# Kernel optimization log

Measured on AMD Instinct MI355X. Metric: run time of the kernel, lower is better.

Reference implementation:

```python
import jax, jax.numpy as jnp
import numpy as np

B, T, D, H = 4, 1024, 1024, 16
TP = 1024
HD = D // H
LN_EPS = 1e-3  # keras LayerNormalization default epsilon


def snac_linear(x, wt, mt):
    # conv1dsnac: w = tanh(wt) * sigmoid(mt), shape [1, nx, nf] -> [nx, nf]
    w = (jnp.tanh(wt) * jax.nn.sigmoid(mt))[0]
    return jnp.einsum('btx,xf->btf', x, w)


def layernorm(x, gamma, beta):
    mu = jnp.mean(x, axis=-1, keepdims=True)
    var = jnp.mean(jnp.square(x - mu), axis=-1, keepdims=True)
    return (x - mu) * jax.lax.rsqrt(var + LN_EPS) * gamma + beta


def setup_inputs() -> dict:
    key = jax.random.key(0)
    ks = jax.random.split(key, 10)
    s = 0.02
    return {
        'input': jax.random.normal(ks[0], (B, T, D), jnp.float32),
        'past': jax.random.normal(ks[1], (B, 2, H, TP, HD), jnp.float32),
        'qkv_wt': jax.random.normal(ks[2], (1, D, 3 * D), jnp.float32) * s,
        'qkv_mt': jax.random.normal(ks[3], (1, D, 3 * D), jnp.float32) * s,
        'merge_wt': jax.random.normal(ks[4], (1, D, D), jnp.float32) * s,
        'merge_mt': jax.random.normal(ks[5], (1, D, D), jnp.float32) * s,
        'ln1_wt': jax.random.normal(ks[6], (1, D, D), jnp.float32) * s,
        'ln1_mt': jax.random.normal(ks[7], (1, D, D), jnp.float32) * s,
        'g1': jnp.ones((D,), jnp.float32), 'b1': jnp.zeros((D,), jnp.float32),
        'g2': jnp.ones((D,), jnp.float32), 'b2': jnp.zeros((D,), jnp.float32),
    }


def reference(input, past, qkv_wt, qkv_mt, merge_wt, merge_mt, ln1_wt, ln1_mt, g1, b1, g2, b2):
    x = input
    xn = layernorm(x, g1, b1)
    c = snac_linear(xn, qkv_wt, qkv_mt)  # [B, T, 3D]
    q, k, v = jnp.split(c, 3, axis=2)
    # split heads -> [B, H, T, HD]
    to_heads = lambda t: t.reshape(B, T, H, HD).transpose(0, 2, 1, 3)
    q, k, v = to_heads(q), to_heads(k), to_heads(v)
    present = jnp.stack([k, v], axis=1)  # [B, 2, H, T, HD]
    pk, pv = past[:, 0], past[:, 1]
    k = jnp.concatenate([pk, k], axis=2)  # [B, H, TP+T, HD]
    v = jnp.concatenate([pv, v], axis=2)
    nd, ns = T, TP + T
    w = jnp.einsum('bhqd,bhkd->bhqk', q, k) * jax.lax.rsqrt(jnp.float32(HD))
    i = jnp.arange(nd)[:, None]
    j = jnp.arange(ns)[None, :]
    m = (i >= j - ns + nd).astype(w.dtype)  # [nd, ns] causal mask incl. past
    w = w * m - jnp.asarray(1e10, w.dtype) * (1 - m)
    msk = jax.nn.softmax(w, axis=-1)  # [B, H, T, TP+T]
    a = jnp.einsum('bhqk,bhkd->bhqd', msk, v)
    ah = a.transpose(0, 2, 1, 3).reshape(B, T, D)  # merge heads
    am = snac_linear(ah, merge_wt, merge_mt)
    xa = x + am
    mlp = snac_linear(layernorm(xa, g2, b2), ln1_wt, ln1_mt)
    xm = xa + mlp
    return xm, present, msk
```

## Files before the change

### kernel.cpp

```cpp
#include <hip/hip_runtime.h>
#include <hip/hip_bf16.h>

typedef _Float16 half8 __attribute__((ext_vector_type(8)));
typedef _Float16 half4v __attribute__((ext_vector_type(4)));
typedef float f32x4 __attribute__((ext_vector_type(4)));

#define DEV static __device__ __forceinline__


typedef __attribute__((address_space(1))) const unsigned int* gas_p;
typedef __attribute__((address_space(3))) unsigned int* las_p;
DEV void glds16(const void* g, void* s) {
  __builtin_amdgcn_global_load_lds((gas_p)g, (las_p)s, 16, 0, 0);
}

__global__ __launch_bounds__(256) void prep_all(const float* __restrict__ qkv_wt,
                                                const float* __restrict__ qkv_mt,
                                                const float* __restrict__ mg_wt,
                                                const float* __restrict__ mg_mt,
                                                const float* __restrict__ l1_wt,
                                                const float* __restrict__ l1_mt,
                                                _Float16* __restrict__ wq,
                                                _Float16* __restrict__ wm,
                                                _Float16* __restrict__ wl) {
  __shared__ float tile[64][65];
  const float *wt, *mt;
  _Float16* out;
  int N, bid;
  if (blockIdx.x < 768) {
    wt = qkv_wt; mt = qkv_mt; out = wq; N = 3072; bid = blockIdx.x;
  } else if (blockIdx.x < 1024) {
    wt = mg_wt; mt = mg_mt; out = wm; N = 1024; bid = blockIdx.x - 768;
  } else {
    wt = l1_wt; mt = l1_mt; out = wl; N = 1024; bid = blockIdx.x - 1024;
  }
  const int ntiles = N >> 6;
  const int nt = bid % ntiles, kt = bid / ntiles;
  const int k0 = kt << 6, n0 = nt << 6;
  const int t = threadIdx.x, r = t >> 2, c0 = (t & 3) << 4;
  const long ibase = (long)(k0 + r) * N + n0 + c0;
#pragma unroll
  for (int j = 0; j < 16; j += 4) {
    float4 a = *(const float4*)(wt + ibase + j);
    float4 b = *(const float4*)(mt + ibase + j);
    tile[r][c0 + j + 0] = tanhf(a.x) / (1.f + __expf(-b.x));
    tile[r][c0 + j + 1] = tanhf(a.y) / (1.f + __expf(-b.y));
    tile[r][c0 + j + 2] = tanhf(a.z) / (1.f + __expf(-b.z));
    tile[r][c0 + j + 3] = tanhf(a.w) / (1.f + __expf(-b.w));
  }
  __syncthreads();
  half8 o0, o1;
#pragma unroll
  for (int j = 0; j < 8; ++j) {
    o0[j] = (_Float16)tile[c0 + j][r];
    o1[j] = (_Float16)tile[c0 + 8 + j][r];
  }
  _Float16* dst = out + (long)(n0 + r) * 1024 + k0 + c0;
  *(half8*)dst = o0;
  *(half8*)(dst + 8) = o1;
}

__global__ __launch_bounds__(256) void kv_prep(const float* __restrict__ past,
                                               const _Float16* __restrict__ vnew,
                                               _Float16* __restrict__ kf,
                                               _Float16* __restrict__ vt) {
  __shared__ float tile[64][65];
  if (blockIdx.x < 4096) {
    const long e = ((long)blockIdx.x * 256 + threadIdx.x) * 4;
    const int b = (int)(e >> 20);
    const int rem = (int)(e & 1048575);
    float4 v = *(const float4*)(past + (long)b * 2097152 + rem);
    half4v o = {(_Float16)v.x, (_Float16)v.y, (_Float16)v.z, (_Float16)v.w};
    const int h = rem >> 16, td = rem & 65535;
    *(half4v*)(kf + (long)(b * 16 + h) * 131072 + td) = o;
    return;
  }
  const int bid = blockIdx.x - 4096;
  const int bh = bid >> 5, kt = bid & 31;
  const int b = bh >> 4, h = bh & 15;
  const int k0 = kt << 6;
  const int t = threadIdx.x, r = t >> 2, c0 = (t & 3) << 4;
  if (k0 < 1024) {
    const float* src = past + (((long)(b * 2 + 1) * 16 + h) * 1024 + (k0 + r)) * 64 + c0;
#pragma unroll
    for (int j = 0; j < 16; j += 4) {
      float4 v = *(const float4*)(src + j);
      tile[r][c0 + j + 0] = v.x;
      tile[r][c0 + j + 1] = v.y;
      tile[r][c0 + j + 2] = v.z;
      tile[r][c0 + j + 3] = v.w;
    }
  } else {
    const _Float16* src = vnew + ((long)bh * 1024 + (k0 - 1024 + r)) * 64 + c0;
    half8 a = *(const half8*)src;
    half8 bq = *(const half8*)(src + 8);
#pragma unroll
    for (int j = 0; j < 8; ++j) {
      tile[r][c0 + j] = (float)a[j];
      tile[r][c0 + 8 + j] = (float)bq[j];
    }
  }
  __syncthreads();
  half8 o0, o1;
#pragma unroll
  for (int j = 0; j < 8; ++j) {
    o0[j] = (_Float16)tile[c0 + j][r];
    o1[j] = (_Float16)tile[c0 + 8 + j][r];
  }
  _Float16* dst = vt + ((long)bh * 64 + r) * 2048 + k0 + c0;
  *(half8*)dst = o0;
  *(half8*)(dst + 8) = o1;
}

__global__ __launch_bounds__(256) void ln_k(const float* __restrict__ x,
                                            const float* __restrict__ g,
                                            const float* __restrict__ be,
                                            _Float16* __restrict__ out) {
  __shared__ float red[4];
  const int row = blockIdx.x, tid = threadIdx.x, l = tid & 63, w = tid >> 6;
  float4 v = *(const float4*)(x + (long)row * 1024 + tid * 4);
  float s = v.x + v.y + v.z + v.w;
#pragma unroll
  for (int o = 32; o > 0; o >>= 1) s += __shfl_down(s, o, 64);
  if (l == 0) red[w] = s;
  __syncthreads();
  const float mu = (red[0] + red[1] + red[2] + red[3]) * (1.f / 1024.f);
  float dx = v.x - mu, dy = v.y - mu, dz = v.z - mu, dw = v.w - mu;
  float ss = dx * dx + dy * dy + dz * dz + dw * dw;
#pragma unroll
  for (int o = 32; o > 0; o >>= 1) ss += __shfl_down(ss, o, 64);
  __syncthreads();
  if (l == 0) red[w] = ss;
  __syncthreads();
  const float var = (red[0] + red[1] + red[2] + red[3]) * (1.f / 1024.f);
  const float rs = rsqrtf(var + 1e-3f);
  float4 gv = *(const float4*)(g + tid * 4);
  float4 bv = *(const float4*)(be + tid * 4);
  half4v o = {(_Float16)(dx * rs * gv.x + bv.x), (_Float16)(dy * rs * gv.y + bv.y),
              (_Float16)(dz * rs * gv.z + bv.z), (_Float16)(dw * rs * gv.w + bv.w)};
  *(half4v*)(out + (long)row * 1024 + tid * 4) = o;
}

template <int BM, int EPI>
__global__ __launch_bounds__(256) void gemm_k(const _Float16* __restrict__ A,
                                              const _Float16* __restrict__ Bt,
                                              int mtiles,
                                              _Float16* __restrict__ e_q,
                                              _Float16* __restrict__ e_k,
                                              _Float16* __restrict__ e_v,
                                              float* __restrict__ e_present,
                                              const float* __restrict__ e_res,
                                              float* __restrict__ e_out) {
  constexpr int FM = BM / 32;
  __shared__ __align__(16) char smem[2 * BM * 128 + 32768];
  char* Bbase = smem + 2 * BM * 128;
  const int tid = threadIdx.x, l = tid & 63, w = tid >> 6;
  const int wm = w >> 1, wn = w & 1;
  const int bm = blockIdx.x % mtiles, bn = blockIdx.x / mtiles;
  const long m0 = (long)bm * BM, n0 = (long)bn * 128;

  f32x4 acc[FM][4];
#pragma unroll
  for (int i = 0; i < FM; ++i)
#pragma unroll
    for (int j = 0; j < 4; ++j) acc[i][j] = (f32x4){0.f, 0.f, 0.f, 0.f};

  auto stage = [&](int b, int kt) {
#pragma unroll
    for (int i = 0; i < FM; ++i) {
      const int cid = i * 256 + tid, row = cid >> 3, u = cid & 7;
      glds16(A + (m0 + row) * 1024 + kt * 64 + ((u ^ (row & 7)) << 3),
             smem + b * BM * 128 + i * 4096 + w * 1024);
    }
#pragma unroll
    for (int i = 0; i < 4; ++i) {
      const int cid = i * 256 + tid, row = cid >> 3, u = cid & 7;
      glds16(Bt + (n0 + row) * 1024 + kt * 64 + ((u ^ (row & 7)) << 3),
             Bbase + b * 16384 + i * 4096 + w * 1024);
    }
  };

  stage(0, 0);
  __syncthreads();
  for (int kt = 0; kt < 16; ++kt) {
    const int cur = kt & 1;
    if (kt < 15) stage(cur ^ 1, kt + 1);
    const char* As = smem + cur * BM * 128;
    const char* Bs = Bbase + cur * 16384;
#pragma unroll
    for (int k2 = 0; k2 < 2; ++k2) {
      const int sl = k2 * 4 + (l >> 4);
      half8 bfr[4];
#pragma unroll
      for (int fn = 0; fn < 4; ++fn) {
        const int rn = wn * 64 + fn * 16 + (l & 15);
        bfr[fn] = *(const half8*)(Bs + rn * 128 + ((sl ^ (rn & 7)) << 4));
      }
#pragma unroll
      for (int fm = 0; fm < FM; ++fm) {
        const int rm = wm * (BM / 2) + fm * 16 + (l & 15);
        const half8 afr = *(const half8*)(As + rm * 128 + ((sl ^ (rm & 7)) << 4));
#pragma unroll
        for (int fn = 0; fn < 4; ++fn)
          acc[fm][fn] = __builtin_amdgcn_mfma_f32_16x16x32_f16(afr, bfr[fn], acc[fm][fn], 0, 0, 0);
      }
    }
    __syncthreads();
  }
#pragma unroll
  for (int fm = 0; fm < FM; ++fm) {
#pragma unroll
    for (int fn = 0; fn < 4; ++fn) {
#pragma unroll
      for (int r = 0; r < 4; ++r) {
        const long row = m0 + wm * (BM / 2) + fm * 16 + (l >> 4) * 4 + r;
        const long col = n0 + fn * 16 + (l & 15) + wn * 64;
        const float v = acc[fm][fn][r];
        if constexpr (EPI == 0) {
          const int b = (int)(row >> 10), t = (int)(row & 1023);
          const int sec = (int)(col >> 10), h = ((int)col >> 6) & 15, hd = (int)col & 63;
          const long bh = b * 16 + h;
          if (sec == 0) {
            e_q[(bh * 1024 + t) * 64 + hd] = (_Float16)v;
          } else if (sec == 1) {
            e_present[(((long)(b * 2) * 16 + h) * 1024 + t) * 64 + hd] = v;
            e_k[(bh * 2048 + 1024 + t) * 64 + hd] = (_Float16)v;
          } else {
            e_present[(((long)(b * 2 + 1) * 16 + h) * 1024 + t) * 64 + hd] = v;
            e_v[(bh * 1024 + t) * 64 + hd] = (_Float16)v;
          }
        } else {
          e_out[row * 1024 + col] = e_res[row * 1024 + col] + v;
        }
      }
    }
  }
}

__global__ __launch_bounds__(256, 4) void attn_k(const _Float16* __restrict__ qg,
                                                 const _Float16* __restrict__ kg,
                                                 const _Float16* __restrict__ vtg,
                                                 float* __restrict__ msk,
                                                 _Float16* __restrict__ ah) {
  __shared__ __align__(16) char smem[40960];
  char* ps_all = smem + 32768;
  const int tid = threadIdx.x, l = tid & 63, w = tid >> 6;
  char* psw = ps_all + w * 2048;
  const int lq = l & 15, hi = l >> 4;

  const int x = blockIdx.x & 7, g = blockIdx.x >> 3;
  const int bh = (g & 7) * 8 + x;
  const int qt = 15 - (g >> 3);
  const int r0 = qt << 6;
  const int nc = (r0 + 1151) >> 6;
  const int rowg0 = r0 + w * 16;

  const _Float16* kb = kg + (long)bh * 131072;
  const _Float16* vb = vtg + (long)bh * 131072;
  float* mskb = msk + ((long)bh * 1024 + rowg0) * 2048;

  half8 qa[2];
  {
    const _Float16* qp = qg + ((long)bh * 1024 + rowg0 + lq) * 64 + hi * 8;
    qa[0] = *(const half8*)qp;
    qa[1] = *(const half8*)(qp + 32);
  }

  auto stageK = [&](int b, int c) {
#pragma unroll
    for (int i = 0; i < 2; ++i) {
      const int cid = i * 256 + tid, row = cid >> 3, u = cid & 7;
      glds16(kb + (long)(c * 64 + row) * 64 + ((u ^ (row & 7)) << 3),
             smem + b * 8192 + i * 4096 + w * 1024);
    }
  };
  auto stageV = [&](int b, int c) {
#pragma unroll
    for (int i = 0; i < 2; ++i) {
      const int cid = i * 256 + tid, row = cid >> 3, u = cid & 7;
      glds16(vb + (long)row * 2048 + c * 64 + ((u ^ (row & 7)) << 3),
             smem + 16384 + b * 8192 + i * 4096 + w * 1024);
    }
  };

  constexpr float C1 = 0.125f * 1.44269504088896341f;
  const int lim = rowg0 + lq + 1024;

  auto qk_tile = [&](const char* ks, f32x4 (&sa)[4]) {
#pragma unroll
    for (int fn = 0; fn < 4; ++fn) sa[fn] = (f32x4){0.f, 0.f, 0.f, 0.f};
#pragma unroll
    for (int k2 = 0; k2 < 2; ++k2) {
      const int sl = k2 * 4 + hi;
      half8 ak[4];
#pragma unroll
      for (int fn = 0; fn < 4; ++fn) {
        const int rn = fn * 16 + lq;
        ak[fn] = *(const half8*)(ks + rn * 128 + ((sl ^ (rn & 7)) << 4));
      }
#pragma unroll
      for (int fn = 0; fn < 4; ++fn)
        sa[fn] = __builtin_amdgcn_mfma_f32_16x16x32_f16(ak[fn], qa[k2], sa[fn], 0, 0, 0);
    }
  };

  float rsum = 0.f;
  stageK(0, 0);
  __syncthreads();
  for (int c = 0; c < nc; ++c) {
    const int cur = c & 1;
    if (c + 1 < nc) stageK(cur ^ 1, c + 1);
    f32x4 sa[4];
    qk_tile(smem + cur * 8192, sa);
    if (c < nc - 1) {
#pragma unroll
      for (int fn = 0; fn < 4; ++fn)
#pragma unroll
        for (int r = 0; r < 4; ++r) rsum += __builtin_amdgcn_exp2f(sa[fn][r] * C1);
    } else {
#pragma unroll
      for (int fn = 0; fn < 4; ++fn)
#pragma unroll
        for (int r = 0; r < 4; ++r) {
          const int col = c * 64 + fn * 16 + hi * 4 + r;
          const float e = __builtin_amdgcn_exp2f(sa[fn][r] * C1);
          rsum += (col <= lim) ? e : 0.f;
        }
    }
    __syncthreads();
  }
  rsum += __shfl_xor(rsum, 16, 64);
  rsum += __shfl_xor(rsum, 32, 64);
  const float c2s = -__builtin_amdgcn_logf(rsum);

  f32x4 pv[4];
#pragma unroll
  for (int j = 0; j < 4; ++j) pv[j] = (f32x4){0.f, 0.f, 0.f, 0.f};
  stageK(0, 0);
  stageV(0, 0);
  __syncthreads();
  for (int c = 0; c < nc; ++c) {
    const int cur = c & 1;
    if (c + 1 < nc) {
      stageK(cur ^ 1, c + 1);
      stageV(cur ^ 1, c + 1);
    }
    f32x4 sa[4];
    qk_tile(smem + cur * 8192, sa);
    const bool bound = (c == nc - 1);
#pragma unroll
    for (int fn = 0; fn < 4; ++fn) {
      float pr[4];
#pragma unroll
      for (int r = 0; r < 4; ++r) {
        float p = __builtin_amdgcn_exp2f(sa[fn][r] * C1 + c2s);
        if (bound) {
          const int col = c * 64 + fn * 16 + hi * 4 + r;
          p = (col <= lim) ? p : 0.f;
        }
        pr[r] = p;
      }
      *(float4*)(mskb + (long)lq * 2048 + c * 64 + fn * 16 + hi * 4) =
          make_float4(pr[0], pr[1], pr[2], pr[3]);
      const half4v hv = {(_Float16)pr[0], (_Float16)pr[1], (_Float16)pr[2],
                         (_Float16)pr[3]};
      const int bc = fn * 32 + hi * 8;
      *(half4v*)(psw + lq * 128 + ((((bc >> 4) ^ (lq & 7)) << 4) | (bc & 15))) = hv;
    }
    __builtin_amdgcn_wave_barrier();
    asm volatile("s_waitcnt lgkmcnt(0)" ::: "memory");
    __builtin_amdgcn_sched_barrier(0);
    const char* vs = smem + 16384 + cur * 8192;
#pragma unroll
    for (int k2p = 0; k2p < 2; ++k2p) {
      const int sl2 = k2p * 4 + hi;
      const half8 pa = *(const half8*)(psw + lq * 128 + ((sl2 ^ (lq & 7)) << 4));
      half8 bv[4];
#pragma unroll
      for (int fn2 = 0; fn2 < 4; ++fn2) {
        const int rd = fn2 * 16 + lq;
        bv[fn2] = *(const half8*)(vs + rd * 128 + ((sl2 ^ (rd & 7)) << 4));
      }
#pragma unroll
      for (int fn2 = 0; fn2 < 4; ++fn2)
        pv[fn2] = __builtin_amdgcn_mfma_f32_16x16x32_f16(pa, bv[fn2], pv[fn2], 0, 0, 0);
    }
    __syncthreads();
  }

  const int ntail = 512 - (nc << 4);
  if (ntail > 0) {
    const float4 z4 = make_float4(0.f, 0.f, 0.f, 0.f);
    for (int row = 0; row < 16; ++row)
      for (int i = l; i < ntail; i += 64)
        *(float4*)(mskb + (long)row * 2048 + nc * 64 + i * 4) = z4;
  }

  const int b_ = bh >> 4, h_ = bh & 15;
  _Float16* ahb = ah + ((long)b_ * 1024 + rowg0) * 1024 + h_ * 64;
#pragma unroll
  for (int fn2 = 0; fn2 < 4; ++fn2)
#pragma unroll
    for (int r = 0; r < 4; ++r)
      ahb[(long)(hi * 4 + r) * 1024 + fn2 * 16 + lq] = (_Float16)pv[fn2][r];
}

extern "C" void kernel_launch(void* const* d_in, const int* in_sizes, int n_in,
                              void* d_out, int out_size, void* d_ws, size_t ws_size,
                              hipStream_t stream) {
  const float* x = (const float*)d_in[0];
  const float* past = (const float*)d_in[1];
  const float* qkv_wt = (const float*)d_in[2];
  const float* qkv_mt = (const float*)d_in[3];
  const float* merge_wt = (const float*)d_in[4];
  const float* merge_mt = (const float*)d_in[5];
  const float* ln1_wt = (const float*)d_in[6];
  const float* ln1_mt = (const float*)d_in[7];
  const float* g1 = (const float*)d_in[8];
  const float* b1 = (const float*)d_in[9];
  const float* g2 = (const float*)d_in[10];
  const float* b2 = (const float*)d_in[11];

  float* out = (float*)d_out;
  float* o_xm = out;
  float* o_present = out + 4194304;
  float* o_msk = out + 4194304 + 8388608;

  char* ws = (char*)d_ws;
  _Float16* wq_t = (_Float16*)(ws + 0);
  _Float16* wm_t = (_Float16*)(ws + 6291456);
  _Float16* wl_t = (_Float16*)(ws + 8388608);
  _Float16* xn   = (_Float16*)(ws + 10485760);
  _Float16* qws  = (_Float16*)(ws + 18874368);
  _Float16* kful = (_Float16*)(ws + 27262976);
  _Float16* vnew = (_Float16*)(ws + 44040192);
  _Float16* vt   = (_Float16*)(ws + 52428800);
  _Float16* ah   = (_Float16*)(ws + 69206016);
  float* xa      = (float*)(ws + 77594624);

  prep_all<<<1280, 256, 0, stream>>>(qkv_wt, qkv_mt, merge_wt, merge_mt, ln1_wt,
                                     ln1_mt, wq_t, wm_t, wl_t);
  ln_k<<<4096, 256, 0, stream>>>(x, g1, b1, xn);
  gemm_k<128, 0><<<768, 256, 0, stream>>>(xn, wq_t, 32, qws, kful, vnew, o_present,
                                          nullptr, nullptr);
  kv_prep<<<6144, 256, 0, stream>>>(past, vnew, kful, vt);
  attn_k<<<1024, 256, 0, stream>>>(qws, kful, vt, o_msk, ah);
  gemm_k<64, 1><<<512, 256, 0, stream>>>(ah, wm_t, 64, nullptr, nullptr, nullptr,
                                         nullptr, x, xa);
  ln_k<<<4096, 256, 0, stream>>>(xa, g2, b2, xn);
  gemm_k<64, 1><<<512, 256, 0, stream>>>(xn, wl_t, 64, nullptr, nullptr, nullptr,
                                         nullptr, xa, o_xm);
}
```

Before: 308.1 us.

## Store residual xa in fp16, widen attention row-sum pass, add MFMA priority hints

Stores the intermediate residual xa as fp16 instead of fp32. The second layernorm reads it as fp16, and the final GEMM epilogue adds the fp16 residual back in fp32. The attention softmax-denominator pass now processes 128-key tiles instead of 64, halving its loop iterations and barriers. s_setprio is raised around the MFMA blocks in the GEMM and attention loops. The fp16 residual cuts memory traffic but loses precision in xa, which feeds both the second layernorm and the final output.

```diff
diff --git a/kernel.cpp b/kernel.cpp
--- a/kernel.cpp
+++ b/kernel.cpp
@@ -112,20 +112,28 @@
   *(half8*)(dst + 8) = o1;
 }
 
-__global__ __launch_bounds__(256) void ln_k(const float* __restrict__ x,
+template <int F16IN>
+__global__ __launch_bounds__(256) void ln_k(const void* __restrict__ xin,
                                             const float* __restrict__ g,
                                             const float* __restrict__ be,
                                             _Float16* __restrict__ out) {
   __shared__ float red[4];
   const int row = blockIdx.x, tid = threadIdx.x, l = tid & 63, w = tid >> 6;
-  float4 v = *(const float4*)(x + (long)row * 1024 + tid * 4);
-  float s = v.x + v.y + v.z + v.w;
+  float v0, v1, v2, v3;
+  if constexpr (F16IN == 0) {
+    float4 v = *(const float4*)((const float*)xin + (long)row * 1024 + tid * 4);
+    v0 = v.x; v1 = v.y; v2 = v.z; v3 = v.w;
+  } else {
+    half4v v = *(const half4v*)((const _Float16*)xin + (long)row * 1024 + tid * 4);
+    v0 = (float)v[0]; v1 = (float)v[1]; v2 = (float)v[2]; v3 = (float)v[3];
+  }
+  float s = v0 + v1 + v2 + v3;
 #pragma unroll
   for (int o = 32; o > 0; o >>= 1) s += __shfl_down(s, o, 64);
   if (l == 0) red[w] = s;
   __syncthreads();
   const float mu = (red[0] + red[1] + red[2] + red[3]) * (1.f / 1024.f);
-  float dx = v.x - mu, dy = v.y - mu, dz = v.z - mu, dw = v.w - mu;
+  float dx = v0 - mu, dy = v1 - mu, dz = v2 - mu, dw = v3 - mu;
   float ss = dx * dx + dy * dy + dz * dz + dw * dw;
 #pragma unroll
   for (int o = 32; o > 0; o >>= 1) ss += __shfl_down(ss, o, 64);
@@ -149,8 +157,8 @@
                                               _Float16* __restrict__ e_k,
                                               _Float16* __restrict__ e_v,
                                               float* __restrict__ e_present,
-                                              const float* __restrict__ e_res,
-                                              float* __restrict__ e_out) {
+                                              const void* __restrict__ e_resv,
+                                              void* __restrict__ e_outv) {
   constexpr int FM = BM / 32;
   __shared__ __align__(16) char smem[2 * BM * 128 + 32768];
   char* Bbase = smem + 2 * BM * 128;
@@ -187,6 +195,7 @@
     if (kt < 15) stage(cur ^ 1, kt + 1);
     const char* As = smem + cur * BM * 128;
     const char* Bs = Bbase + cur * 16384;
+    __builtin_amdgcn_s_setprio(1);
 #pragma unroll
     for (int k2 = 0; k2 < 2; ++k2) {
       const int sl = k2 * 4 + (l >> 4);
@@ -205,6 +214,7 @@
           acc[fm][fn] = __builtin_amdgcn_mfma_f32_16x16x32_f16(afr, bfr[fn], acc[fm][fn], 0, 0, 0);
       }
     }
+    __builtin_amdgcn_s_setprio(0);
     __syncthreads();
   }
 #pragma unroll
@@ -229,8 +239,12 @@
             e_present[(((long)(b * 2 + 1) * 16 + h) * 1024 + t) * 64 + hd] = v;
             e_v[(bh * 1024 + t) * 64 + hd] = (_Float16)v;
           }
+        } else if constexpr (EPI == 1) {
+          ((_Float16*)e_outv)[row * 1024 + col] =
+              (_Float16)(((const float*)e_resv)[row * 1024 + col] + v);
         } else {
-          e_out[row * 1024 + col] = e_res[row * 1024 + col] + v;
+          ((float*)e_outv)[row * 1024 + col] =
+              (float)((const _Float16*)e_resv)[row * 1024 + col] + v;
         }
       }
     }
@@ -252,7 +266,6 @@
   const int bh = (g & 7) * 8 + x;
   const int qt = 15 - (g >> 3);
   const int r0 = qt << 6;
-  const int nc = (r0 + 1151) >> 6;
   const int rowg0 = r0 + w * 16;
 
   const _Float16* kb = kg + (long)bh * 131072;
@@ -266,6 +279,65 @@
     qa[1] = *(const half8*)(qp + 32);
   }
 
+  constexpr float C1 = 0.125f * 1.44269504088896341f;
+  const int lim = rowg0 + lq + 1024;
+
+  const int nc1 = (r0 + 1215) >> 7;
+  auto stageK128 = [&](int b, int c) {
+#pragma unroll
+    for (int i = 0; i < 4; ++i) {
+      const int cid = i * 256 + tid, row = cid >> 3, u = cid & 7;
+      glds16(kb + (long)(c * 128 + row) * 64 + ((u ^ (row & 7)) << 3),
+             smem + b * 16384 + i * 4096 + w * 1024);
+    }
+  };
+  float rsum = 0.f;
+  stageK128(0, 0);
+  __syncthreads();
+  for (int c = 0; c < nc1; ++c) {
+    const int cur = c & 1;
+    if (c + 1 < nc1) stageK128(cur ^ 1, c + 1);
+    const char* ks = smem + cur * 16384;
+    f32x4 sa[8];
+#pragma unroll
+    for (int fn = 0; fn < 8; ++fn) sa[fn] = (f32x4){0.f, 0.f, 0.f, 0.f};
+    __builtin_amdgcn_s_setprio(1);
+#pragma unroll
+    for (int k2 = 0; k2 < 2; ++k2) {
+      const int sl = k2 * 4 + hi;
+      half8 ak[8];
+#pragma unroll
+      for (int fn = 0; fn < 8; ++fn) {
+        const int rn = fn * 16 + lq;
+        ak[fn] = *(const half8*)(ks + rn * 128 + ((sl ^ (rn & 7)) << 4));
+      }
+#pragma unroll
+      for (int fn = 0; fn < 8; ++fn)
+        sa[fn] = __builtin_amdgcn_mfma_f32_16x16x32_f16(ak[fn], qa[k2], sa[fn], 0, 0, 0);
+    }
+    __builtin_amdgcn_s_setprio(0);
+    if (c < nc1 - 1) {
+#pragma unroll
+      for (int fn = 0; fn < 8; ++fn)
+#pragma unroll
+        for (int r = 0; r < 4; ++r) rsum += __builtin_amdgcn_exp2f(sa[fn][r] * C1);
+    } else {
+#pragma unroll
+      for (int fn = 0; fn < 8; ++fn)
+#pragma unroll
+        for (int r = 0; r < 4; ++r) {
+          const int col = c * 128 + fn * 16 + hi * 4 + r;
+          const float e = __builtin_amdgcn_exp2f(sa[fn][r] * C1);
+          rsum += (col <= lim) ? e : 0.f;
+        }
+    }
+    __syncthreads();
+  }
+  rsum += __shfl_xor(rsum, 16, 64);
+  rsum += __shfl_xor(rsum, 32, 64);
+  const float c2s = -__builtin_amdgcn_logf(rsum);
+
+  const int nc = (r0 + 1151) >> 6;
   auto stageK = [&](int b, int c) {
 #pragma unroll
     for (int i = 0; i < 2; ++i) {
@@ -283,59 +355,10 @@
     }
   };
 
-  constexpr float C1 = 0.125f * 1.44269504088896341f;
-  const int lim = rowg0 + lq + 1024;
-
-  auto qk_tile = [&](const char* ks, f32x4 (&sa)[4]) {
-#pragma unroll
-    for (int fn = 0; fn < 4; ++fn) sa[fn] = (f32x4){0.f, 0.f, 0.f, 0.f};
-#pragma unroll
-    for (int k2 = 0; k2 < 2; ++k2) {
-      const int sl = k2 * 4 + hi;
-      half8 ak[4];
-#pragma unroll
-      for (int fn = 0; fn < 4; ++fn) {
-        const int rn = fn * 16 + lq;
-        ak[fn] = *(const half8*)(ks + rn * 128 + ((sl ^ (rn & 7)) << 4));
-      }
-#pragma unroll
-      for (int fn = 0; fn < 4; ++fn)
-        sa[fn] = __builtin_amdgcn_mfma_f32_16x16x32_f16(ak[fn], qa[k2], sa[fn], 0, 0, 0);
-    }
-  };
-
-  float rsum = 0.f;
-  stageK(0, 0);
-  __syncthreads();
-  for (int c = 0; c < nc; ++c) {
-    const int cur = c & 1;
-    if (c + 1 < nc) stageK(cur ^ 1, c + 1);
-    f32x4 sa[4];
-    qk_tile(smem + cur * 8192, sa);
-    if (c < nc - 1) {
-#pragma unroll
-      for (int fn = 0; fn < 4; ++fn)
-#pragma unroll
-        for (int r = 0; r < 4; ++r) rsum += __builtin_amdgcn_exp2f(sa[fn][r] * C1);
-    } else {
-#pragma unroll
-      for (int fn = 0; fn < 4; ++fn)
-#pragma unroll
-        for (int r = 0; r < 4; ++r) {
-          const int col = c * 64 + fn * 16 + hi * 4 + r;
-          const float e = __builtin_amdgcn_exp2f(sa[fn][r] * C1);
-          rsum += (col <= lim) ? e : 0.f;
-        }
-    }
-    __syncthreads();
-  }
-  rsum += __shfl_xor(rsum, 16, 64);
-  rsum += __shfl_xor(rsum, 32, 64);
-  const float c2s = -__builtin_amdgcn_logf(rsum);
-
   f32x4 pv[4];
 #pragma unroll
   for (int j = 0; j < 4; ++j) pv[j] = (f32x4){0.f, 0.f, 0.f, 0.f};
+  __syncthreads();
   stageK(0, 0);
   stageV(0, 0);
   __syncthreads();
@@ -345,8 +368,25 @@
       stageK(cur ^ 1, c + 1);
       stageV(cur ^ 1, c + 1);
     }
+    const char* ks = smem + cur * 8192;
     f32x4 sa[4];
-    qk_tile(smem + cur * 8192, sa);
+#pragma unroll
+    for (int fn = 0; fn < 4; ++fn) sa[fn] = (f32x4){0.f, 0.f, 0.f, 0.f};
+    __builtin_amdgcn_s_setprio(1);
+#pragma unroll
+    for (int k2 = 0; k2 < 2; ++k2) {
+      const int sl = k2 * 4 + hi;
+      half8 ak[4];
+#pragma unroll
+      for (int fn = 0; fn < 4; ++fn) {
+        const int rn = fn * 16 + lq;
+        ak[fn] = *(const half8*)(ks + rn * 128 + ((sl ^ (rn & 7)) << 4));
+      }
+#pragma unroll
+      for (int fn = 0; fn < 4; ++fn)
+        sa[fn] = __builtin_amdgcn_mfma_f32_16x16x32_f16(ak[fn], qa[k2], sa[fn], 0, 0, 0);
+    }
+    __builtin_amdgcn_s_setprio(0);
     const bool bound = (c == nc - 1);
 #pragma unroll
     for (int fn = 0; fn < 4; ++fn) {
@@ -371,6 +411,7 @@
     asm volatile("s_waitcnt lgkmcnt(0)" ::: "memory");
     __builtin_amdgcn_sched_barrier(0);
     const char* vs = smem + 16384 + cur * 8192;
+    __builtin_amdgcn_s_setprio(1);
 #pragma unroll
     for (int k2p = 0; k2p < 2; ++k2p) {
       const int sl2 = k2p * 4 + hi;
@@ -385,6 +426,7 @@
       for (int fn2 = 0; fn2 < 4; ++fn2)
         pv[fn2] = __builtin_amdgcn_mfma_f32_16x16x32_f16(pa, bv[fn2], pv[fn2], 0, 0, 0);
     }
+    __builtin_amdgcn_s_setprio(0);
     __syncthreads();
   }
 
@@ -436,18 +478,18 @@
   _Float16* vnew = (_Float16*)(ws + 44040192);
   _Float16* vt   = (_Float16*)(ws + 52428800);
   _Float16* ah   = (_Float16*)(ws + 69206016);
-  float* xa      = (float*)(ws + 77594624);
+  _Float16* xa   = (_Float16*)(ws + 77594624);
 
   prep_all<<<1280, 256, 0, stream>>>(qkv_wt, qkv_mt, merge_wt, merge_mt, ln1_wt,
                                      ln1_mt, wq_t, wm_t, wl_t);
-  ln_k<<<4096, 256, 0, stream>>>(x, g1, b1, xn);
+  ln_k<0><<<4096, 256, 0, stream>>>(x, g1, b1, xn);
   gemm_k<128, 0><<<768, 256, 0, stream>>>(xn, wq_t, 32, qws, kful, vnew, o_present,
                                           nullptr, nullptr);
   kv_prep<<<6144, 256, 0, stream>>>(past, vnew, kful, vt);
   attn_k<<<1024, 256, 0, stream>>>(qws, kful, vt, o_msk, ah);
   gemm_k<64, 1><<<512, 256, 0, stream>>>(ah, wm_t, 64, nullptr, nullptr, nullptr,
                                          nullptr, x, xa);
-  ln_k<<<4096, 256, 0, stream>>>(xa, g2, b2, xn);
-  gemm_k<64, 1><<<512, 256, 0, stream>>>(xn, wl_t, 64, nullptr, nullptr, nullptr,
+  ln_k<1><<<4096, 256, 0, stream>>>(xa, g2, b2, xn);
+  gemm_k<64, 2><<<512, 256, 0, stream>>>(xn, wl_t, 64, nullptr, nullptr, nullptr,
                                          nullptr, xa, o_xm);
 }
```

Result: faster. 289.0 us (-6.2%).
